# Kernel optimization log

Hardware: AMD Instinct MI355X
Metric: run time of the kernel (lower is better)

Reference implementation:

```python
import jax, jax.numpy as jnp
import numpy as np

N_NODES = 100000
N_EDGES = 500000
E_HID = 64
IN_DIM = 192  # r_hidden + 2*t_hidden
NEG_SLOPE = 0.01


def setup_inputs() -> dict:
    key = jax.random.key(0)
    ks = jax.random.split(key, 16)
    s_in = 1.0 / np.sqrt(IN_DIM)
    s_e = 1.0 / np.sqrt(E_HID)
    inp = {
        "x_e": jax.random.normal(ks[0], (N_NODES, E_HID), dtype=jnp.float32),
        "x_r": jax.random.normal(ks[1], (N_EDGES, IN_DIM), dtype=jnp.float32),
        "edge_index": jax.random.randint(ks[2], (2, N_EDGES), 0, N_NODES, dtype=jnp.int64),
        "rel_size": jnp.arange(N_EDGES, dtype=jnp.int64),
        "Wr": jax.random.uniform(ks[3], (E_HID, IN_DIM), jnp.float32, -s_in, s_in),
        "br": jax.random.uniform(ks[4], (E_HID,), jnp.float32, -s_in, s_in),
        "Wr1": jax.random.uniform(ks[5], (E_HID, IN_DIM), jnp.float32, -s_in, s_in),
        "br1": jax.random.uniform(ks[6], (E_HID,), jnp.float32, -s_in, s_in),
        "Wr2": jax.random.uniform(ks[7], (E_HID, IN_DIM), jnp.float32, -s_in, s_in),
        "br2": jax.random.uniform(ks[8], (E_HID,), jnp.float32, -s_in, s_in),
        "ah": jax.random.uniform(ks[9], (E_HID,), jnp.float32, -s_e, s_e),
        "ah1": jax.random.uniform(ks[10], (E_HID,), jnp.float32, -s_e, s_e),
        "at": jax.random.uniform(ks[11], (E_HID,), jnp.float32, -s_e, s_e),
        "ar1": jax.random.uniform(ks[12], (E_HID,), jnp.float32, -s_e, s_e),
        "ar2": jax.random.uniform(ks[13], (E_HID,), jnp.float32, -s_e, s_e),
        "ar3": jax.random.uniform(ks[14], (E_HID,), jnp.float32, -s_e, s_e),
    }
    return inp


def _gat_block(x_e, x_r, idx, rel_size, W, b, a_node, a_rel, num_nodes):
    # e_r = w_r(x_r): [E, e_hid]
    e_r = x_r @ W.T + b
    # attention logits per edge: a_node . x_e[idx] + a_rel . e_r
    logits = x_e[idx] @ a_node + e_r @ a_rel  # [E]
    lr = jnp.where(logits > 0, logits, NEG_SLOPE * logits)  # leaky_relu
    # segment softmax over destination segments (idx)
    m = jax.ops.segment_max(lr, idx, num_segments=num_nodes)
    ex = jnp.exp(lr - m[idx])
    s = jax.ops.segment_sum(ex, idx, num_segments=num_nodes)
    alpha = ex / (s[idx] + 1e-16)
    # spmm: out[n] = sum_{e: idx[e]==n} alpha[e] * e_r[rel_size[e]]
    agg = jax.ops.segment_sum(alpha[:, None] * e_r[rel_size], idx, num_segments=num_nodes)
    return x_e + jax.nn.relu(agg)


def reference(x_e, x_r, edge_index, rel_size, Wr, br, Wr1, br1, Wr2, br2,
              ah, ah1, at, ar1, ar2, ar3):
    n = x_e.shape[0]
    h, t = edge_index[0], edge_index[1]
    x_e = _gat_block(x_e, x_r, h, rel_size, Wr, br, ah, ar1, n)
    x_e = _gat_block(x_e, x_r, t, rel_size, Wr1, br1, at, ar2, n)
    x_e = _gat_block(x_e, x_r, h, rel_size, Wr2, br2, ah1, ar3, n)
    return x_e
```

## Files before the change

kernel.cpp:

```cpp
#include <hip/hip_runtime.h>
#include <hip/hip_bf16.h>

typedef __attribute__((ext_vector_type(8))) short short8;
typedef __attribute__((ext_vector_type(4))) float f32x4;

#define DEV __device__ __forceinline__

#define BARRIER() do { asm volatile("s_waitcnt lgkmcnt(0)" ::: "memory"); \
                       __builtin_amdgcn_s_barrier(); \
                       __builtin_amdgcn_sched_barrier(0); } while (0)

DEV unsigned short f2bf(float f) {
    unsigned u = __float_as_uint(f);
    u += 0x7FFFu + ((u >> 16) & 1u);
    return (unsigned short)(u >> 16);
}
DEV float bf2f(unsigned short h) { return __uint_as_float(((unsigned)h) << 16); }
DEV unsigned pk2(float lo, float hi) {
    float2 f; f.x = lo; f.y = hi;
    __hip_bfloat162 h = __float22bfloat162_rn(f);
    unsigned r; __builtin_memcpy(&r, &h, 4);
    return r;
}
union S8 { short8 s; unsigned u[4]; };

__global__ __launch_bounds__(512, 2) void gemm_k(
    const float* __restrict__ xr,
    const float* __restrict__ W0, const float* __restrict__ W1, const float* __restrict__ W2,
    const float* __restrict__ b0, const float* __restrict__ b1, const float* __restrict__ b2,
    unsigned short* __restrict__ er,
    int E, int ntiles, int K)
{
    __shared__ __align__(16) unsigned short ShBuf[192 * 192];
    unsigned short* Ws = ShBuf;
    const int t = threadIdx.x;
    const int w = t >> 6, l = t & 63, l15 = l & 15, lg = l >> 4;
    const int cgrp = w & 3, rh = w >> 2;
    const int srow = t >> 3, sq = t & 7;

#pragma unroll
    for (int j = 0; j < 9; ++j) {
        const int c = j * 512 + t;
        const int gc = c / 24, pos = c - gc * 24;
        const int m = gc >> 6, row = gc & 63;
        const float* Wm = (m == 0) ? W0 : ((m == 1) ? W1 : W2);
        const float4 u0 = *(const float4*)(Wm + row * 192 + pos * 8);
        const float4 u1 = *(const float4*)(Wm + row * 192 + pos * 8 + 4);
        S8 o;
        o.u[0] = pk2(u0.x, u0.y); o.u[1] = pk2(u0.z, u0.w);
        o.u[2] = pk2(u1.x, u1.y); o.u[3] = pk2(u1.z, u1.w);
        const unsigned byte = (unsigned)(gc * 384 + pos * 16);
        *(short8*)((char*)Ws + (byte ^ ((gc & 7) << 4))) = o.s;
    }

    const int G = gridDim.x;
    float4 nv[6];
    if (blockIdx.x < ntiles) {
        const long e = (long)blockIdx.x * 64 + srow;
        const bool ok = e < E;
        const float* sp = xr + e * (long)K + sq * 24;
#pragma unroll
        for (int r = 0; r < 6; ++r)
            nv[r] = ok ? *(const float4*)(sp + r * 4) : make_float4(0.f, 0.f, 0.f, 0.f);
    }

    BARRIER();
    short8 bfr[3][6];
#pragma unroll
    for (int i = 0; i < 3; ++i) {
        const int gc = (cgrp * 3 + i) * 16 + l15;
#pragma unroll
        for (int ks = 0; ks < 6; ++ks) {
            const unsigned byte = (unsigned)(gc * 384 + ks * 64 + lg * 16);
            bfr[i][ks] = *(const short8*)((const char*)Ws + (byte ^ ((gc & 7) << 4)));
        }
    }
    BARRIER();

    int p = 0;
    for (int tile = blockIdx.x; tile < ntiles; tile += G, p ^= 1) {
        const long e0 = (long)tile * 64;
        char* Ab = (char*)(ShBuf + p * 64 * 192);
        {
            const unsigned swz = (unsigned)((srow & 7) << 4);
            S8 o0, o1, o2;
            o0.u[0] = pk2(nv[0].x, nv[0].y); o0.u[1] = pk2(nv[0].z, nv[0].w);
            o0.u[2] = pk2(nv[1].x, nv[1].y); o0.u[3] = pk2(nv[1].z, nv[1].w);
            o1.u[0] = pk2(nv[2].x, nv[2].y); o1.u[1] = pk2(nv[2].z, nv[2].w);
            o1.u[2] = pk2(nv[3].x, nv[3].y); o1.u[3] = pk2(nv[3].z, nv[3].w);
            o2.u[0] = pk2(nv[4].x, nv[4].y); o2.u[1] = pk2(nv[4].z, nv[4].w);
            o2.u[2] = pk2(nv[5].x, nv[5].y); o2.u[3] = pk2(nv[5].z, nv[5].w);
            const unsigned byte0 = (unsigned)(srow * 384 + sq * 48);
            *(short8*)(Ab + ((byte0 +  0) ^ swz)) = o0.s;
            *(short8*)(Ab + ((byte0 + 16) ^ swz)) = o1.s;
            *(short8*)(Ab + ((byte0 + 32) ^ swz)) = o2.s;
        }
        {
            const int nxt = tile + G;
            if (nxt < ntiles) {
                const long e = (long)nxt * 64 + srow;
                const bool ok = e < E;
                const float* sp = xr + e * (long)K + sq * 24;
#pragma unroll
                for (int r = 0; r < 6; ++r)
                    nv[r] = ok ? *(const float4*)(sp + r * 4)
                               : make_float4(0.f, 0.f, 0.f, 0.f);
            }
        }
        BARRIER();
        f32x4 acc[2][3];
#pragma unroll
        for (int rt = 0; rt < 2; ++rt)
#pragma unroll
            for (int i = 0; i < 3; ++i) acc[rt][i] = (f32x4)(0.f);
#pragma unroll
        for (int ks = 0; ks < 6; ++ks) {
            short8 af[2];
#pragma unroll
            for (int rt = 0; rt < 2; ++rt) {
                const int row = rh * 32 + rt * 16 + l15;
                const unsigned byte = (unsigned)(row * 384 + ks * 64 + lg * 16);
                af[rt] = *(const short8*)((const char*)Ab + (byte ^ ((row & 7) << 4)));
            }
#pragma unroll
            for (int i = 0; i < 3; ++i)
#pragma unroll
                for (int rt = 0; rt < 2; ++rt)
                    acc[rt][i] = __builtin_amdgcn_mfma_f32_16x16x32_bf16(bfr[i][ks], af[rt], acc[rt][i], 0, 0, 0);
        }
#pragma unroll
        for (int i = 0; i < 3; ++i) {
            const int ct = cgrp * 3 + i, m = ct >> 2;
            const int cb_ = ((ct & 3) << 4) + (lg << 2);
            const float* bp = (m == 0) ? b0 : ((m == 1) ? b1 : b2);
            const float4 bb = *(const float4*)(bp + cb_);
            const int fb = ct * 16 + (lg << 2);
#pragma unroll
            for (int rt = 0; rt < 2; ++rt) {
                const int edge = rh * 32 + rt * 16 + l15;
                const long ee = e0 + edge;
                if (ee < E) {
                    uint2 pkv;
                    pkv.x = pk2(acc[rt][i][0] + bb.x, acc[rt][i][1] + bb.y);
                    pkv.y = pk2(acc[rt][i][2] + bb.z, acc[rt][i][3] + bb.w);
                    *(uint2*)(er + (size_t)ee * 192 + fb) = pkv;
                }
            }
        }
    }
}

__global__ __launch_bounds__(256) void count2_k(const int* __restrict__ h,
                                                const int* __restrict__ tt,
                                                int* __restrict__ deg, int E, int N)
{
    const int e = blockIdx.x * 256 + threadIdx.x;
    if (e >= E) return;
    atomicAdd(&deg[h[e]], 1);
    atomicAdd(&deg[N + tt[e]], 1);
}

__global__ __launch_bounds__(256) void scan1_k(const int* __restrict__ deg,
                                               int* __restrict__ incl,
                                               int* __restrict__ bsum, int M)
{
    __shared__ int buf[256];
    const int tid = threadIdx.x;
    const int n = blockIdx.x * 256 + tid;
    buf[tid] = (n < M) ? deg[n] : 0;
    __syncthreads();
    for (int d = 1; d < 256; d <<= 1) {
        int v = (tid >= d) ? buf[tid - d] : 0;
        __syncthreads();
        buf[tid] += v;
        __syncthreads();
    }
    if (n < M) incl[n] = buf[tid];
    if (tid == 255) bsum[blockIdx.x] = buf[255];
}

__global__ __launch_bounds__(256) void scan2_k(int* __restrict__ bsum, int nb)
{
    __shared__ int wsum[4];
    const int tid = threadIdx.x, l = tid & 63, wv = tid >> 6;
    int base = 0;
    for (int start = 0; start < nb; start += 1024) {
        const int i0 = start + tid * 4;
        int v0 = 0, v1 = 0, v2 = 0, v3 = 0;
        if (i0 < nb)     v0 = bsum[i0];
        if (i0 + 1 < nb) v1 = bsum[i0 + 1];
        if (i0 + 2 < nb) v2 = bsum[i0 + 2];
        if (i0 + 3 < nb) v3 = bsum[i0 + 3];
        const int tsum = v0 + v1 + v2 + v3;
        int sc = tsum;
#pragma unroll
        for (int d = 1; d < 64; d <<= 1) {
            const int o = __shfl_up(sc, d);
            if (l >= d) sc += o;
        }
        if (l == 63) wsum[wv] = sc;
        __syncthreads();
        int woff = base;
        for (int q = 0; q < wv; ++q) woff += wsum[q];
        int run = woff + sc - tsum;
        run += v0; if (i0 < nb)     bsum[i0] = run;
        run += v1; if (i0 + 1 < nb) bsum[i0 + 1] = run;
        run += v2; if (i0 + 2 < nb) bsum[i0 + 2] = run;
        run += v3; if (i0 + 3 < nb) bsum[i0 + 3] = run;
        base += wsum[0] + wsum[1] + wsum[2] + wsum[3];
        __syncthreads();
    }
}

__global__ __launch_bounds__(256) void off_k(const int* __restrict__ deg,
                                             const int* __restrict__ incl,
                                             const int* __restrict__ bsum,
                                             int* __restrict__ off,
                                             int* __restrict__ cur, int M, int tot)
{
    const int n = blockIdx.x * 256 + threadIdx.x;
    if (n < M) {
        const int prev = (blockIdx.x > 0) ? bsum[blockIdx.x - 1] : 0;
        const int o = prev + incl[n] - deg[n];
        off[n] = o;
        cur[n] = o;
    }
    if (n == 0) off[M] = tot;
}

__global__ __launch_bounds__(256) void fill2_k(const int* __restrict__ h,
                                               const int* __restrict__ tt,
                                               int* __restrict__ cur,
                                               int* __restrict__ elist, int E, int N)
{
    const int e = blockIdx.x * 256 + threadIdx.x;
    if (e >= E) return;
    const int p = atomicAdd(&cur[h[e]], 1);
    elist[p] = e;
    const int p2 = atomicAdd(&cur[N + tt[e]], 1);
    elist[p2] = e;
}

__global__ __launch_bounds__(256, 6) void gat3_k(
    const int* __restrict__ off, const int* __restrict__ elist,
    const unsigned short* __restrict__ er,
    const float* __restrict__ xe, float* __restrict__ out,
    const float* __restrict__ an0, const float* __restrict__ an1,
    const float* __restrict__ an2,
    const float* __restrict__ ar0, const float* __restrict__ ar1,
    const float* __restrict__ ar2, int N)
{
    __shared__ float sm[4][8][64];
    const int wv = threadIdx.x >> 6;
    const int node = blockIdx.x * 4 + wv;
    if (node >= N) return;
    const int l = threadIdx.x & 63;
    const int g = l >> 3, q = l & 7;

    const int h0 = off[node], h1 = off[node + 1];
    const int t0 = off[N + node], t1 = off[N + node + 1];
    float x = xe[(size_t)node * 64 + l];

    if ((h1 - h0) <= 8 && (t1 - t0) <= 8) {
        const bool vh = g < (h1 - h0), vt = g < (t1 - t0);
        const int eh = vh ? elist[h0 + g] : 0;
        const int et = vt ? elist[t0 + g] : 0;
        short8 w0, w1, w2;
        w0 = vh ? *(const short8*)(er + (size_t)eh * 192 +       q * 8) : (short8)(short)0;
        w1 = vt ? *(const short8*)(er + (size_t)et * 192 +  64 + q * 8) : (short8)(short)0;
        w2 = vh ? *(const short8*)(er + (size_t)eh * 192 + 128 + q * 8) : (short8)(short)0;

#pragma unroll
        for (int b = 0; b < 3; ++b) {
            const float* anb = (b == 0) ? an0 : ((b == 1) ? an1 : an2);
            const float* arb = (b == 0) ? ar0 : ((b == 1) ? ar1 : ar2);
            const bool val = (b == 1) ? vt : vh;
            const short8 vv = (b == 0) ? w0 : ((b == 1) ? w1 : w2);

            float pv = x * anb[l];
#pragma unroll
            for (int d = 1; d < 64; d <<= 1) pv += __shfl_xor(pv, d);

            const float4 a1 = *(const float4*)(arb + q * 8);
            const float4 a2 = *(const float4*)(arb + q * 8 + 4);
            float dd = bf2f((unsigned short)vv[0]) * a1.x
                     + bf2f((unsigned short)vv[1]) * a1.y
                     + bf2f((unsigned short)vv[2]) * a1.z
                     + bf2f((unsigned short)vv[3]) * a1.w
                     + bf2f((unsigned short)vv[4]) * a2.x
                     + bf2f((unsigned short)vv[5]) * a2.y
                     + bf2f((unsigned short)vv[6]) * a2.z
                     + bf2f((unsigned short)vv[7]) * a2.w;
            dd += __shfl_xor(dd, 1);
            dd += __shfl_xor(dd, 2);
            dd += __shfl_xor(dd, 4);

            const float lr = pv + dd;
            const float lv = lr > 0.f ? lr : 0.01f * lr;
            float mt = val ? lv : -1e30f;
            mt = fmaxf(mt, __shfl_xor(mt, 8));
            mt = fmaxf(mt, __shfl_xor(mt, 16));
            mt = fmaxf(mt, __shfl_xor(mt, 32));
            const float wg = val ? __expf(lv - mt) : 0.f;
            float s = wg;
            s += __shfl_xor(s, 8);
            s += __shfl_xor(s, 16);
            s += __shfl_xor(s, 32);

            f32x4 aA, aB;
            aA[0] = wg * bf2f((unsigned short)vv[0]);
            aA[1] = wg * bf2f((unsigned short)vv[1]);
            aA[2] = wg * bf2f((unsigned short)vv[2]);
            aA[3] = wg * bf2f((unsigned short)vv[3]);
            aB[0] = wg * bf2f((unsigned short)vv[4]);
            aB[1] = wg * bf2f((unsigned short)vv[5]);
            aB[2] = wg * bf2f((unsigned short)vv[6]);
            aB[3] = wg * bf2f((unsigned short)vv[7]);
            *(f32x4*)&sm[wv][g][q * 8] = aA;
            *(f32x4*)&sm[wv][g][q * 8 + 4] = aB;
            asm volatile("s_waitcnt lgkmcnt(0)" ::: "memory");
            __builtin_amdgcn_sched_barrier(0);
            float a = 0.f;
#pragma unroll
            for (int gg = 0; gg < 8; ++gg) a += sm[wv][gg][l];
            asm volatile("s_waitcnt lgkmcnt(0)" ::: "memory");
            __builtin_amdgcn_sched_barrier(0);

            x += fmaxf(a / (s + 1e-16f), 0.f);
        }
    } else {
#pragma unroll
        for (int b = 0; b < 3; ++b) {
            const float* anb = (b == 0) ? an0 : ((b == 1) ? an1 : an2);
            const float* arb = (b == 0) ? ar0 : ((b == 1) ? ar1 : ar2);
            const int cb = b * 64;
            const int s0 = (b == 1) ? t0 : h0, s1 = (b == 1) ? t1 : h1;

            float pv = x * anb[l];
#pragma unroll
            for (int d = 1; d < 64; d <<= 1) pv += __shfl_xor(pv, d);
            const float4 a1 = *(const float4*)(arb + q * 8);
            const float4 a2 = *(const float4*)(arb + q * 8 + 4);

            float m = -1e30f, s = 0.f;
            f32x4 aA = (f32x4)(0.f), aB = (f32x4)(0.f);
            for (int j = s0; j < s1; j += 8) {
                const int jj = j + g;
                if (jj < s1) {
                    const int e = elist[jj];
                    const short8 v = *(const short8*)(er + (size_t)e * 192 + cb + q * 8);
                    float dd = bf2f((unsigned short)v[0]) * a1.x
                             + bf2f((unsigned short)v[1]) * a1.y
                             + bf2f((unsigned short)v[2]) * a1.z
                             + bf2f((unsigned short)v[3]) * a1.w
                             + bf2f((unsigned short)v[4]) * a2.x
                             + bf2f((unsigned short)v[5]) * a2.y
                             + bf2f((unsigned short)v[6]) * a2.z
                             + bf2f((unsigned short)v[7]) * a2.w;
                    dd += __shfl_xor(dd, 1);
                    dd += __shfl_xor(dd, 2);
                    dd += __shfl_xor(dd, 4);
                    const float lg_ = pv + dd;
                    const float lv = lg_ > 0.f ? lg_ : 0.01f * lg_;
                    const float nm = fmaxf(m, lv);
                    const float rs = __expf(m - nm);
                    const float wg = __expf(lv - nm);
                    s = s * rs + wg;
                    aA[0] = aA[0] * rs + wg * bf2f((unsigned short)v[0]);
                    aA[1] = aA[1] * rs + wg * bf2f((unsigned short)v[1]);
                    aA[2] = aA[2] * rs + wg * bf2f((unsigned short)v[2]);
                    aA[3] = aA[3] * rs + wg * bf2f((unsigned short)v[3]);
                    aB[0] = aB[0] * rs + wg * bf2f((unsigned short)v[4]);
                    aB[1] = aB[1] * rs + wg * bf2f((unsigned short)v[5]);
                    aB[2] = aB[2] * rs + wg * bf2f((unsigned short)v[6]);
                    aB[3] = aB[3] * rs + wg * bf2f((unsigned short)v[7]);
                    m = nm;
                }
            }
            float mt = m;
            mt = fmaxf(mt, __shfl_xor(mt, 8));
            mt = fmaxf(mt, __shfl_xor(mt, 16));
            mt = fmaxf(mt, __shfl_xor(mt, 32));
            const float rs2 = __expf(m - mt);
            s *= rs2;
            s += __shfl_xor(s, 8);
            s += __shfl_xor(s, 16);
            s += __shfl_xor(s, 32);
#pragma unroll
            for (int c = 0; c < 4; ++c) { aA[c] *= rs2; aB[c] *= rs2; }
            *(f32x4*)&sm[wv][g][q * 8] = aA;
            *(f32x4*)&sm[wv][g][q * 8 + 4] = aB;
            asm volatile("s_waitcnt lgkmcnt(0)" ::: "memory");
            __builtin_amdgcn_sched_barrier(0);
            float a = 0.f;
#pragma unroll
            for (int gg = 0; gg < 8; ++gg) a += sm[wv][gg][l];
            asm volatile("s_waitcnt lgkmcnt(0)" ::: "memory");
            __builtin_amdgcn_sched_barrier(0);

            x += fmaxf(a / (s + 1e-16f), 0.f);
        }
    }
    out[(size_t)node * 64 + l] = x;
}

extern "C" void kernel_launch(void* const* d_in, const int* in_sizes, int n_in,
                              void* d_out, int out_size, void* d_ws, size_t ws_size,
                              hipStream_t stream)
{
    const float* xe  = (const float*)d_in[0];
    const float* xr  = (const float*)d_in[1];
    const int*   eix = (const int*)d_in[2];
    const float* Wr  = (const float*)d_in[4];
    const float* br  = (const float*)d_in[5];
    const float* Wr1 = (const float*)d_in[6];
    const float* br1 = (const float*)d_in[7];
    const float* Wr2 = (const float*)d_in[8];
    const float* br2 = (const float*)d_in[9];
    const float* ah  = (const float*)d_in[10];
    const float* ah1 = (const float*)d_in[11];
    const float* at_ = (const float*)d_in[12];
    const float* ar1 = (const float*)d_in[13];
    const float* ar2 = (const float*)d_in[14];
    const float* ar3 = (const float*)d_in[15];

    const int E = in_sizes[3];
    const int N = in_sizes[0] / 64;
    const int K = in_sizes[1] / E;
    const int M = 2 * N;
    float* out = (float*)d_out;

    char* p = (char*)d_ws;
    auto carve = [&](size_t bytes) -> void* {
        void* r = (void*)p;
        p += (bytes + 255) & ~(size_t)255;
        return r;
    };
    const int nb = (M + 255) / 256;
    unsigned short* er = (unsigned short*)carve((size_t)(E + 64) * 192 * 2);
    int* off = (int*)carve((size_t)(M + 1) * 4);
    int* elist = (int*)carve((size_t)2 * E * 4);
    int* deg = (int*)carve((size_t)M * 4);
    int* incl = (int*)carve((size_t)M * 4);
    int* cur = (int*)carve((size_t)M * 4);
    int* bsum = (int*)carve((size_t)nb * 4);
    (void)ws_size;

    const int Eg = (E + 255) / 256;
    const int ng = (N + 3) / 4;
    const int ntiles = (E + 63) / 64;
    const int ggrid = ntiles < 512 ? ntiles : 512;

    hipMemsetAsync(deg, 0, (size_t)M * 4, stream);
    count2_k<<<Eg, 256, 0, stream>>>(eix, eix + E, deg, E, N);
    scan1_k<<<nb, 256, 0, stream>>>(deg, incl, bsum, M);
    scan2_k<<<1, 256, 0, stream>>>(bsum, nb);
    off_k<<<nb, 256, 0, stream>>>(deg, incl, bsum, off, cur, M, 2 * E);
    fill2_k<<<Eg, 256, 0, stream>>>(eix, eix + E, cur, elist, E, N);

    gemm_k<<<ggrid, 512, 0, stream>>>(xr, Wr, Wr1, Wr2, br, br1, br2,
                                      er, E, ntiles, K);

    gat3_k<<<ng, 256, 0, stream>>>(off, elist, er, xe, out,
                                   ah, at_, ah1, ar1, ar2, ar3, N);
}
```

Measured before the change: 356.3 us.

## Make GAT kernel persistent with multi-stage software prefetch of node data

Turns the per-node GAT aggregation kernel into a grid-stride persistent kernel with 1024 blocks. Offsets, edge ids, node features and edge-embedding rows for upcoming nodes are loaded several iterations ahead, so the dependent gather chain off→elist→er overlaps with compute. Occupancy hint drops from 6 to 4 to leave room for the extra prefetch registers. The cost is that fewer waves are resident, and the loads for high-degree nodes on the fallback path are wasted.

```diff
diff --git a/kernel.cpp b/kernel.cpp
--- a/kernel.cpp
+++ b/kernel.cpp
@@ -241,7 +241,9 @@
     elist[p2] = e;
 }
 
-__global__ __launch_bounds__(256, 6) void gat3_k(
+struct ERt { short8 w0, w1, w2; };
+
+__global__ __launch_bounds__(256, 4) void gat3_k(
     const int* __restrict__ off, const int* __restrict__ elist,
     const unsigned short* __restrict__ er,
     const float* __restrict__ xe, float* __restrict__ out,
@@ -252,156 +254,196 @@
 {
     __shared__ float sm[4][8][64];
     const int wv = threadIdx.x >> 6;
-    const int node = blockIdx.x * 4 + wv;
-    if (node >= N) return;
     const int l = threadIdx.x & 63;
     const int g = l >> 3, q = l & 7;
-
-    const int h0 = off[node], h1 = off[node + 1];
-    const int t0 = off[N + node], t1 = off[N + node + 1];
-    float x = xe[(size_t)node * 64 + l];
-
-    if ((h1 - h0) <= 8 && (t1 - t0) <= 8) {
-        const bool vh = g < (h1 - h0), vt = g < (t1 - t0);
-        const int eh = vh ? elist[h0 + g] : 0;
-        const int et = vt ? elist[t0 + g] : 0;
-        short8 w0, w1, w2;
-        w0 = vh ? *(const short8*)(er + (size_t)eh * 192 +       q * 8) : (short8)(short)0;
-        w1 = vt ? *(const short8*)(er + (size_t)et * 192 +  64 + q * 8) : (short8)(short)0;
-        w2 = vh ? *(const short8*)(er + (size_t)eh * 192 + 128 + q * 8) : (short8)(short)0;
-
-#pragma unroll
-        for (int b = 0; b < 3; ++b) {
-            const float* anb = (b == 0) ? an0 : ((b == 1) ? an1 : an2);
-            const float* arb = (b == 0) ? ar0 : ((b == 1) ? ar1 : ar2);
-            const bool val = (b == 1) ? vt : vh;
-            const short8 vv = (b == 0) ? w0 : ((b == 1) ? w1 : w2);
-
-            float pv = x * anb[l];
-#pragma unroll
-            for (int d = 1; d < 64; d <<= 1) pv += __shfl_xor(pv, d);
-
-            const float4 a1 = *(const float4*)(arb + q * 8);
-            const float4 a2 = *(const float4*)(arb + q * 8 + 4);
-            float dd = bf2f((unsigned short)vv[0]) * a1.x
-                     + bf2f((unsigned short)vv[1]) * a1.y
-                     + bf2f((unsigned short)vv[2]) * a1.z
-                     + bf2f((unsigned short)vv[3]) * a1.w
-                     + bf2f((unsigned short)vv[4]) * a2.x
-                     + bf2f((unsigned short)vv[5]) * a2.y
-                     + bf2f((unsigned short)vv[6]) * a2.z
-                     + bf2f((unsigned short)vv[7]) * a2.w;
-            dd += __shfl_xor(dd, 1);
-            dd += __shfl_xor(dd, 2);
-            dd += __shfl_xor(dd, 4);
-
-            const float lr = pv + dd;
-            const float lv = lr > 0.f ? lr : 0.01f * lr;
-            float mt = val ? lv : -1e30f;
-            mt = fmaxf(mt, __shfl_xor(mt, 8));
-            mt = fmaxf(mt, __shfl_xor(mt, 16));
-            mt = fmaxf(mt, __shfl_xor(mt, 32));
-            const float wg = val ? __expf(lv - mt) : 0.f;
-            float s = wg;
-            s += __shfl_xor(s, 8);
-            s += __shfl_xor(s, 16);
-            s += __shfl_xor(s, 32);
-
-            f32x4 aA, aB;
-            aA[0] = wg * bf2f((unsigned short)vv[0]);
-            aA[1] = wg * bf2f((unsigned short)vv[1]);
-            aA[2] = wg * bf2f((unsigned short)vv[2]);
-            aA[3] = wg * bf2f((unsigned short)vv[3]);
-            aB[0] = wg * bf2f((unsigned short)vv[4]);
-            aB[1] = wg * bf2f((unsigned short)vv[5]);
-            aB[2] = wg * bf2f((unsigned short)vv[6]);
-            aB[3] = wg * bf2f((unsigned short)vv[7]);
-            *(f32x4*)&sm[wv][g][q * 8] = aA;
-            *(f32x4*)&sm[wv][g][q * 8 + 4] = aB;
-            asm volatile("s_waitcnt lgkmcnt(0)" ::: "memory");
-            __builtin_amdgcn_sched_barrier(0);
-            float a = 0.f;
-#pragma unroll
-            for (int gg = 0; gg < 8; ++gg) a += sm[wv][gg][l];
-            asm volatile("s_waitcnt lgkmcnt(0)" ::: "memory");
-            __builtin_amdgcn_sched_barrier(0);
-
-            x += fmaxf(a / (s + 1e-16f), 0.f);
-        }
-    } else {
-#pragma unroll
-        for (int b = 0; b < 3; ++b) {
-            const float* anb = (b == 0) ? an0 : ((b == 1) ? an1 : an2);
-            const float* arb = (b == 0) ? ar0 : ((b == 1) ? ar1 : ar2);
-            const int cb = b * 64;
-            const int s0 = (b == 1) ? t0 : h0, s1 = (b == 1) ? t1 : h1;
-
-            float pv = x * anb[l];
-#pragma unroll
-            for (int d = 1; d < 64; d <<= 1) pv += __shfl_xor(pv, d);
-            const float4 a1 = *(const float4*)(arb + q * 8);
-            const float4 a2 = *(const float4*)(arb + q * 8 + 4);
-
-            float m = -1e30f, s = 0.f;
-            f32x4 aA = (f32x4)(0.f), aB = (f32x4)(0.f);
-            for (int j = s0; j < s1; j += 8) {
-                const int jj = j + g;
-                if (jj < s1) {
-                    const int e = elist[jj];
-                    const short8 v = *(const short8*)(er + (size_t)e * 192 + cb + q * 8);
-                    float dd = bf2f((unsigned short)v[0]) * a1.x
-                             + bf2f((unsigned short)v[1]) * a1.y
-                             + bf2f((unsigned short)v[2]) * a1.z
-                             + bf2f((unsigned short)v[3]) * a1.w
-                             + bf2f((unsigned short)v[4]) * a2.x
-                             + bf2f((unsigned short)v[5]) * a2.y
-                             + bf2f((unsigned short)v[6]) * a2.z
-                             + bf2f((unsigned short)v[7]) * a2.w;
-                    dd += __shfl_xor(dd, 1);
-                    dd += __shfl_xor(dd, 2);
-                    dd += __shfl_xor(dd, 4);
-                    const float lg_ = pv + dd;
-                    const float lv = lg_ > 0.f ? lg_ : 0.01f * lg_;
-                    const float nm = fmaxf(m, lv);
-                    const float rs = __expf(m - nm);
-                    const float wg = __expf(lv - nm);
-                    s = s * rs + wg;
-                    aA[0] = aA[0] * rs + wg * bf2f((unsigned short)v[0]);
-                    aA[1] = aA[1] * rs + wg * bf2f((unsigned short)v[1]);
-                    aA[2] = aA[2] * rs + wg * bf2f((unsigned short)v[2]);
-                    aA[3] = aA[3] * rs + wg * bf2f((unsigned short)v[3]);
-                    aB[0] = aB[0] * rs + wg * bf2f((unsigned short)v[4]);
-                    aB[1] = aB[1] * rs + wg * bf2f((unsigned short)v[5]);
-                    aB[2] = aB[2] * rs + wg * bf2f((unsigned short)v[6]);
-                    aB[3] = aB[3] * rs + wg * bf2f((unsigned short)v[7]);
-                    m = nm;
+    const long stride = (long)gridDim.x * 4;
+    long n = (long)blockIdx.x * 4 + wv;
+    if (n >= N) return;
+
+    auto ldOff = [&](long nn) -> int4 {
+        if (nn >= N) nn = N - 1;
+        int4 o;
+        o.x = off[nn];     o.y = off[nn + 1];
+        o.z = off[N + nn]; o.w = off[N + nn + 1];
+        return o;
+    };
+    auto ldIds = [&](const int4& o) -> int2 {
+        const int dh = o.y - o.x, dt = o.w - o.z;
+        int2 r;
+        const int gh = (g < dh) ? g : (dh - 1);
+        const int gt = (g < dt) ? g : (dt - 1);
+        r.x = (dh > 0) ? elist[o.x + gh] : 0;
+        r.y = (dt > 0) ? elist[o.z + gt] : 0;
+        return r;
+    };
+    auto ldEr = [&](const int2& ids) -> ERt {
+        ERt r;
+        r.w0 = *(const short8*)(er + (size_t)ids.x * 192 +       q * 8);
+        r.w1 = *(const short8*)(er + (size_t)ids.y * 192 +  64 + q * 8);
+        r.w2 = *(const short8*)(er + (size_t)ids.x * 192 + 128 + q * 8);
+        return r;
+    };
+    auto ldX = [&](long nn) -> float {
+        if (nn >= N) nn = N - 1;
+        return xe[(size_t)nn * 64 + l];
+    };
+
+    int4 offA = ldOff(n);
+    int2 idsA = ldIds(offA);
+    float xA = ldX(n);
+    ERt erA = ldEr(idsA);
+    int4 offB = ldOff(n + stride);
+    int2 idsB = ldIds(offB);
+    float xB = ldX(n + stride);
+    int4 offC = ldOff(n + 2 * stride);
+
+    for (; n < N; n += stride) {
+        const int4 o = offA;
+        const ERt wr = erA;
+        float x = xA;
+        offA = offB; idsA = idsB; xA = xB;
+        erA = ldEr(idsA);
+        offB = offC;
+        idsB = ldIds(offB);
+        xB = ldX(n + 2 * stride);
+        offC = ldOff(n + 3 * stride);
+
+        const int dh = o.y - o.x, dt = o.w - o.z;
+        if (dh <= 8 && dt <= 8) {
+            const bool vh = g < dh, vt = g < dt;
+#pragma unroll
+            for (int b = 0; b < 3; ++b) {
+                const float* anb = (b == 0) ? an0 : ((b == 1) ? an1 : an2);
+                const float* arb = (b == 0) ? ar0 : ((b == 1) ? ar1 : ar2);
+                const bool val = (b == 1) ? vt : vh;
+                const short8 vv = (b == 0) ? wr.w0 : ((b == 1) ? wr.w1 : wr.w2);
+
+                float pv = x * anb[l];
+#pragma unroll
+                for (int d = 1; d < 64; d <<= 1) pv += __shfl_xor(pv, d);
+
+                const float4 a1 = *(const float4*)(arb + q * 8);
+                const float4 a2 = *(const float4*)(arb + q * 8 + 4);
+                float dd = bf2f((unsigned short)vv[0]) * a1.x
+                         + bf2f((unsigned short)vv[1]) * a1.y
+                         + bf2f((unsigned short)vv[2]) * a1.z
+                         + bf2f((unsigned short)vv[3]) * a1.w
+                         + bf2f((unsigned short)vv[4]) * a2.x
+                         + bf2f((unsigned short)vv[5]) * a2.y
+                         + bf2f((unsigned short)vv[6]) * a2.z
+                         + bf2f((unsigned short)vv[7]) * a2.w;
+                dd += __shfl_xor(dd, 1);
+                dd += __shfl_xor(dd, 2);
+                dd += __shfl_xor(dd, 4);
+
+                const float lr = pv + dd;
+                const float lv = lr > 0.f ? lr : 0.01f * lr;
+                float mt = val ? lv : -1e30f;
+                mt = fmaxf(mt, __shfl_xor(mt, 8));
+                mt = fmaxf(mt, __shfl_xor(mt, 16));
+                mt = fmaxf(mt, __shfl_xor(mt, 32));
+                const float wg = val ? __expf(lv - mt) : 0.f;
+                float s = wg;
+                s += __shfl_xor(s, 8);
+                s += __shfl_xor(s, 16);
+                s += __shfl_xor(s, 32);
+
+                f32x4 aA, aB;
+                aA[0] = wg * bf2f((unsigned short)vv[0]);
+                aA[1] = wg * bf2f((unsigned short)vv[1]);
+                aA[2] = wg * bf2f((unsigned short)vv[2]);
+                aA[3] = wg * bf2f((unsigned short)vv[3]);
+                aB[0] = wg * bf2f((unsigned short)vv[4]);
+                aB[1] = wg * bf2f((unsigned short)vv[5]);
+                aB[2] = wg * bf2f((unsigned short)vv[6]);
+                aB[3] = wg * bf2f((unsigned short)vv[7]);
+                *(f32x4*)&sm[wv][g][q * 8] = aA;
+                *(f32x4*)&sm[wv][g][q * 8 + 4] = aB;
+                asm volatile("s_waitcnt lgkmcnt(0)" ::: "memory");
+                __builtin_amdgcn_sched_barrier(0);
+                float a = 0.f;
+#pragma unroll
+                for (int gg = 0; gg < 8; ++gg) a += sm[wv][gg][l];
+                asm volatile("s_waitcnt lgkmcnt(0)" ::: "memory");
+                __builtin_amdgcn_sched_barrier(0);
+
+                x += fmaxf(a / (s + 1e-16f), 0.f);
+            }
+        } else {
+#pragma unroll
+            for (int b = 0; b < 3; ++b) {
+                const float* anb = (b == 0) ? an0 : ((b == 1) ? an1 : an2);
+                const float* arb = (b == 0) ? ar0 : ((b == 1) ? ar1 : ar2);
+                const int cb = b * 64;
+                const int s0 = (b == 1) ? o.z : o.x, s1 = (b == 1) ? o.w : o.y;
+
+                float pv = x * anb[l];
+#pragma unroll
+                for (int d = 1; d < 64; d <<= 1) pv += __shfl_xor(pv, d);
+                const float4 a1 = *(const float4*)(arb + q * 8);
+                const float4 a2 = *(const float4*)(arb + q * 8 + 4);
+
+                float m = -1e30f, s = 0.f;
+                f32x4 aA = (f32x4)(0.f), aB = (f32x4)(0.f);
+                for (int j = s0; j < s1; j += 8) {
+                    const int jj = j + g;
+                    if (jj < s1) {
+                        const int e = elist[jj];
+                        const short8 v = *(const short8*)(er + (size_t)e * 192 + cb + q * 8);
+                        float dd = bf2f((unsigned short)v[0]) * a1.x
+                                 + bf2f((unsigned short)v[1]) * a1.y
+                                 + bf2f((unsigned short)v[2]) * a1.z
+                                 + bf2f((unsigned short)v[3]) * a1.w
+                                 + bf2f((unsigned short)v[4]) * a2.x
+                                 + bf2f((unsigned short)v[5]) * a2.y
+                                 + bf2f((unsigned short)v[6]) * a2.z
+                                 + bf2f((unsigned short)v[7]) * a2.w;
+                        dd += __shfl_xor(dd, 1);
+                        dd += __shfl_xor(dd, 2);
+                        dd += __shfl_xor(dd, 4);
+                        const float lg_ = pv + dd;
+                        const float lv = lg_ > 0.f ? lg_ : 0.01f * lg_;
+                        const float nm = fmaxf(m, lv);
+                        const float rs = __expf(m - nm);
+                        const float wg = __expf(lv - nm);
+                        s = s * rs + wg;
+                        aA[0] = aA[0] * rs + wg * bf2f((unsigned short)v[0]);
+                        aA[1] = aA[1] * rs + wg * bf2f((unsigned short)v[1]);
+                        aA[2] = aA[2] * rs + wg * bf2f((unsigned short)v[2]);
+                        aA[3] = aA[3] * rs + wg * bf2f((unsigned short)v[3]);
+                        aB[0] = aB[0] * rs + wg * bf2f((unsigned short)v[4]);
+                        aB[1] = aB[1] * rs + wg * bf2f((unsigned short)v[5]);
+                        aB[2] = aB[2] * rs + wg * bf2f((unsigned short)v[6]);
+                        aB[3] = aB[3] * rs + wg * bf2f((unsigned short)v[7]);
+                        m = nm;
+                    }
                 }
+                float mt = m;
+                mt = fmaxf(mt, __shfl_xor(mt, 8));
+                mt = fmaxf(mt, __shfl_xor(mt, 16));
+                mt = fmaxf(mt, __shfl_xor(mt, 32));
+                const float rs2 = __expf(m - mt);
+                s *= rs2;
+                s += __shfl_xor(s, 8);
+                s += __shfl_xor(s, 16);
+                s += __shfl_xor(s, 32);
+#pragma unroll
+                for (int c = 0; c < 4; ++c) { aA[c] *= rs2; aB[c] *= rs2; }
+                *(f32x4*)&sm[wv][g][q * 8] = aA;
+                *(f32x4*)&sm[wv][g][q * 8 + 4] = aB;
+                asm volatile("s_waitcnt lgkmcnt(0)" ::: "memory");
+                __builtin_amdgcn_sched_barrier(0);
+                float a = 0.f;
+#pragma unroll
+                for (int gg = 0; gg < 8; ++gg) a += sm[wv][gg][l];
+                asm volatile("s_waitcnt lgkmcnt(0)" ::: "memory");
+                __builtin_amdgcn_sched_barrier(0);
+
+                x += fmaxf(a / (s + 1e-16f), 0.f);
             }
-            float mt = m;
-            mt = fmaxf(mt, __shfl_xor(mt, 8));
-            mt = fmaxf(mt, __shfl_xor(mt, 16));
-            mt = fmaxf(mt, __shfl_xor(mt, 32));
-            const float rs2 = __expf(m - mt);
-            s *= rs2;
-            s += __shfl_xor(s, 8);
-            s += __shfl_xor(s, 16);
-            s += __shfl_xor(s, 32);
-#pragma unroll
-            for (int c = 0; c < 4; ++c) { aA[c] *= rs2; aB[c] *= rs2; }
-            *(f32x4*)&sm[wv][g][q * 8] = aA;
-            *(f32x4*)&sm[wv][g][q * 8 + 4] = aB;
-            asm volatile("s_waitcnt lgkmcnt(0)" ::: "memory");
-            __builtin_amdgcn_sched_barrier(0);
-            float a = 0.f;
-#pragma unroll
-            for (int gg = 0; gg < 8; ++gg) a += sm[wv][gg][l];
-            asm volatile("s_waitcnt lgkmcnt(0)" ::: "memory");
-            __builtin_amdgcn_sched_barrier(0);
-
-            x += fmaxf(a / (s + 1e-16f), 0.f);
-        }
-    }
-    out[(size_t)node * 64 + l] = x;
+        }
+        out[(size_t)n * 64 + l] = x;
+    }
 }
 
 extern "C" void kernel_launch(void* const* d_in, const int* in_sizes, int n_in,
@@ -447,9 +489,9 @@
     (void)ws_size;
 
     const int Eg = (E + 255) / 256;
-    const int ng = (N + 3) / 4;
     const int ntiles = (E + 63) / 64;
     const int ggrid = ntiles < 512 ? ntiles : 512;
+    const int ngat = 1024;
 
     hipMemsetAsync(deg, 0, (size_t)M * 4, stream);
     count2_k<<<Eg, 256, 0, stream>>>(eix, eix + E, deg, E, N);
@@ -461,6 +503,6 @@
     gemm_k<<<ggrid, 512, 0, stream>>>(xr, Wr, Wr1, Wr2, br, br1, br2,
                                       er, E, ntiles, K);
 
-    gat3_k<<<ng, 256, 0, stream>>>(off, elist, er, xe, out,
-                                   ah, at_, ah1, ar1, ar2, ar3, N);
-}
+    gat3_k<<<ngat, 256, 0, stream>>>(off, elist, er, xe, out,
+                                     ah, at_, ah1, ar1, ar2, ar3, N);
+}
```

New measurement: 378.7 us. 1.06x slower.
